# Optimization experiments

Measured on AMD Instinct MI355X. Metric: run time of the kernel, lower is better.

Reference implementation:

```python
import jax, jax.numpy as jnp
import numpy as np

NPOINT = 1024
K = 16
D_MODEL = 512
EPS = 1e-5


def _fps(xyz, npoint):
    # deterministic farthest point sampling (start at index 0)
    B, N, _ = xyz.shape
    def step(carry, _):
        dist, far = carry                                   # [B,N], [B]
        cent = jnp.take_along_axis(xyz, far[:, None, None], axis=1)  # [B,1,3]
        d = jnp.sum((xyz - cent) ** 2, axis=-1)             # [B,N]
        dist = jnp.minimum(dist, d)
        nxt = jnp.argmax(dist, axis=-1).astype(jnp.int32)
        return (dist, nxt), far
    init = (jnp.full((B, N), 1e10, xyz.dtype), jnp.zeros((B,), jnp.int32))
    _, idx = jax.lax.scan(step, init, None, length=npoint)
    return jnp.transpose(idx)                                # [B, npoint]


def _bn_relu(x, gamma, beta):
    # BatchNorm (training-mode batch stats, biased var) over all axes but channel-last
    axes = tuple(range(x.ndim - 1))
    mu = jnp.mean(x, axes, keepdims=True)
    var = jnp.var(x, axes, keepdims=True)
    return jax.nn.relu((x - mu) * jax.lax.rsqrt(var + EPS) * gamma + beta)


def _forward(xyz, feat, w1, b1, g1, bt1, fc1_w, fc1_b, wq, wk, wv, fc2_w, fc2_b,
             w2, b2, g2, bt2):
    B, N, C = feat.shape
    fps_idx = _fps(xyz, NPOINT)                              # [B,S]
    new_xyz = jnp.take_along_axis(xyz, fps_idx[:, :, None], axis=1)  # [B,S,3]
    # kNN of sampled centers against all points: squared distances [B,S,N]
    d = (jnp.sum(new_xyz ** 2, -1)[:, :, None]
         + jnp.sum(xyz ** 2, -1)[:, None, :]
         - 2.0 * jnp.einsum('bsc,bnc->bsn', new_xyz, xyz))
    _, knn_idx = jax.lax.top_k(-d, K)                        # [B,S,K]
    grouped = jnp.take_along_axis(
        feat, knn_idx.reshape(B, -1)[:, :, None], axis=1
    ).reshape(B, NPOINT, K, C)                               # [B,S,K,C]
    # mlp1: 1x1 conv + BN + ReLU (channel-last)
    x = _bn_relu(grouped @ w1.T + b1, g1, bt1)
    # TransformerBlock: local self-attention over the K neighbors
    pre = x
    h = x @ fc1_w.T + fc1_b                                  # [B,S,K,D]
    q, kk, v = h @ wq.T, h @ wk.T, h @ wv.T
    attn = jax.nn.softmax(
        jnp.einsum('bsnd,bsmd->bsnm', q, kk) / np.sqrt(D_MODEL), axis=-1)
    res = jnp.einsum('bsnm,bsmd->bsnd', attn, v)
    x = res @ fc2_w.T + fc2_b + pre                          # [B,S,K,C]
    # mlp2: 1x1 conv + BN + ReLU -> out_channel
    x = _bn_relu(x @ w2.T + b2, g2, bt2)                     # [B,S,K,out]
    new_feat = jnp.max(x, axis=2)                            # max-pool over neighbors
    return new_xyz, new_feat


def setup_inputs() -> dict:
    key = jax.random.key(0)
    ks = jax.random.split(key, 12)
    s = 0.02
    return {
        'xyz': jax.random.uniform(ks[0], (8, 4096, 3), jnp.float32),
        'feat': jax.random.normal(ks[1], (8, 4096, 64), jnp.float32),
        'w1': jax.random.normal(ks[2], (64, 64), jnp.float32) * s,
        'b1': jnp.zeros((64,), jnp.float32),
        'g1': jnp.ones((64,), jnp.float32),
        'bt1': jnp.zeros((64,), jnp.float32),
        'fc1_w': jax.random.normal(ks[3], (512, 64), jnp.float32) * s,
        'fc1_b': jnp.zeros((512,), jnp.float32),
        'wq': jax.random.normal(ks[4], (512, 512), jnp.float32) * s,
        'wk': jax.random.normal(ks[5], (512, 512), jnp.float32) * s,
        'wv': jax.random.normal(ks[6], (512, 512), jnp.float32) * s,
        'fc2_w': jax.random.normal(ks[7], (64, 512), jnp.float32) * s,
        'fc2_b': jnp.zeros((64,), jnp.float32),
        'w2': jax.random.normal(ks[8], (128, 64), jnp.float32) * s,
        'b2': jnp.zeros((128,), jnp.float32),
        'g2': jnp.ones((128,), jnp.float32),
        'bt2': jnp.zeros((128,), jnp.float32),
    }


def reference(xyz, feat, w1, b1, g1, bt1, fc1_w, fc1_b, wq, wk, wv, fc2_w, fc2_b,
              w2, b2, g2, bt2):
    return _forward(xyz, feat, w1, b1, g1, bt1, fc1_w, fc1_b, wq, wk, wv,
                    fc2_w, fc2_b, w2, b2, g2, bt2)
```

## Files before the change

kernel.cpp:

```cpp
#include <hip/hip_runtime.h>

#define EPSBN 1e-5f
#define INVSQ 0.04419417382415922f

#define WS_KNN_IDX   32768u
#define WS_X1        1048576u
#define WS_BNP1      34603008u
#define WS_BN1S      34865152u
#define WS_BNP2      34865664u
#define WS_BN2S      35914240u
#define WS_A         35915264u
#define WS_B         36046336u
#define WS_QB        36177408u
#define WS_KB        36179456u
#define WS_WC        36181504u
#define WS_G         36312576u
#define WS_ZT        36328960u
#define WS_U         36345344u
#define WS_W         36345600u
#define WS_TB        36345856u
#define WS_CC        36346112u
#define WS_PTS4      36346368u
#define WS_FPSPD     36870656u
#define WS_FPSC4     37001728u

__global__ __launch_bounds__(256) void pack_kernel(const float* __restrict__ xyz,
                                                   float4* __restrict__ pts4) {
  int id = blockIdx.x * 256 + threadIdx.x;
  float x = xyz[id * 3 + 0], y = xyz[id * 3 + 1], z = xyz[id * 3 + 2];
  float pp = __fadd_rn(__fadd_rn(__fmul_rn(x, x), __fmul_rn(y, y)), __fmul_rn(z, z));
  pts4[id] = make_float4(x, y, z, pp);
}

#define FPS_REDSTEP(CTRL)                                                              \
  {                                                                                    \
    unsigned lo2 = (unsigned)__builtin_amdgcn_update_dpp(0, (int)klo, CTRL, 0xF, 0xF, true); \
    unsigned hi2 = (unsigned)__builtin_amdgcn_update_dpp(0, (int)khi, CTRL, 0xF, 0xF, true); \
    bool tk = (hi2 > khi) || (hi2 == khi && lo2 > klo);                                \
    khi = tk ? hi2 : khi; klo = tk ? lo2 : klo;                                        \
  }

__device__ __forceinline__ void fps_chunk_body(unsigned char* smem, const float4* __restrict__ pts4,
                                               float* __restrict__ out_xyz,
                                               float* __restrict__ fps_pd,
                                               float4* __restrict__ fps_c4,
                                               int it0, int b, int t) {
  float4* spts = reinterpret_cast<float4*>(smem);
  float4* cent = reinterpret_cast<float4*>(smem + 65536);
  unsigned long long* red = reinterpret_cast<unsigned long long*>(smem + 73728);
  const int lane = t & 63, wid = t >> 6;
  const float4* pb = pts4 + (size_t)b * 4096;
  float px[16], py[16], pz[16], pd[16];
  if (it0 == 0) {
#pragma unroll
    for (int i = 0; i < 16; ++i) {
      int j = i * 256 + t;
      float4 p = pb[j];
      spts[j] = p;
      px[i] = p.x; py[i] = p.y; pz[i] = p.z; pd[i] = 1e10f;
    }
  } else {
#pragma unroll
    for (int i = 0; i < 16; ++i) {
      int j = i * 256 + t;
      float4 p = pb[j];
      spts[j] = p;
      px[i] = p.x; py[i] = p.y; pz[i] = p.z;
      pd[i] = fps_pd[i * 2048 + b * 256 + t];
    }
  }
  __syncthreads();
  float4 c4 = (it0 == 0) ? spts[0] : fps_c4[b];
  for (int it = it0; it < it0 + 512; ++it) {
    if (t == 0) cent[it - it0] = c4;
    float bv = -1.0f; int bj = 0;
#pragma unroll
    for (int i = 0; i < 16; ++i) {
      float dx = __fsub_rn(px[i], c4.x);
      float dy = __fsub_rn(py[i], c4.y);
      float dz = __fsub_rn(pz[i], c4.z);
      float d = __fadd_rn(__fadd_rn(__fmul_rn(dx, dx), __fmul_rn(dy, dy)), __fmul_rn(dz, dz));
      float nd = fminf(pd[i], d);
      pd[i] = nd;
      bool g = nd > bv;
      bv = g ? nd : bv;
      bj = g ? (i * 256 + t) : bj;
    }
    unsigned klo = 4095u - (unsigned)bj;
    unsigned khi = __float_as_uint(bv);
    FPS_REDSTEP(0x111)
    FPS_REDSTEP(0x112)
    FPS_REDSTEP(0x114)
    FPS_REDSTEP(0x118)
    FPS_REDSTEP(0x142)
    FPS_REDSTEP(0x143)
    unsigned wlo = (unsigned)__builtin_amdgcn_readlane((int)klo, 63);
    unsigned whi = (unsigned)__builtin_amdgcn_readlane((int)khi, 63);
    const int par = it & 1;
    if (lane == 0) red[par * 4 + wid] = (((unsigned long long)whi) << 32) | wlo;
    __syncthreads();
    const ulonglong2* r2 = reinterpret_cast<const ulonglong2*>(&red[par * 4]);
    ulonglong2 ka = r2[0];
    ulonglong2 kb2 = r2[1];
    unsigned long long m0 = (ka.x > ka.y) ? ka.x : ka.y;
    unsigned long long m1 = (kb2.x > kb2.y) ? kb2.x : kb2.y;
    unsigned long long k0 = (m0 > m1) ? m0 : m1;
    int jw = 4095 - (int)(unsigned)(k0 & 0xFFFFFFFFull);
    c4 = spts[jw];
  }
#pragma unroll
  for (int i = 0; i < 16; ++i) fps_pd[i * 2048 + b * 256 + t] = pd[i];
  if (t == 0) fps_c4[b] = c4;
  __syncthreads();
  for (int o = t; o < 1536; o += 256) {
    int j = o / 3;
    int c = o - 3 * j;
    out_xyz[(size_t)b * 3072 + (size_t)it0 * 3 + o] = (&cent[j].x)[c];
  }
}

__device__ __forceinline__ void knn_role_body(const float4* __restrict__ pts4,
                                              const float* __restrict__ out_xyz,
                                              int* __restrict__ knn_idx,
                                              int knn_c0, int blk, int t) {
  const int lane = t & 63;
  const int wv2 = (blk << 2) | (t >> 6);
  const int b = wv2 >> 9;
  const int center = b * 1024 + knn_c0 + (wv2 & 511);
  const float4* P = pts4 + (size_t)b * 4096;
  const float cx = out_xyz[(size_t)center * 3 + 0];
  const float cy = out_xyz[(size_t)center * 3 + 1];
  const float cz = out_xyz[(size_t)center * 3 + 2];
  const float cc2 = __fadd_rn(__fadd_rn(__fmul_rn(cx, cx), __fmul_rn(cy, cy)), __fmul_rn(cz, cz));
  float ldd[16]; int ldi[16];
#pragma unroll
  for (int q = 0; q < 16; ++q) { ldd[q] = 3.4e38f; ldi[q] = 0x7fffffff; }
  for (int i = 0; i < 64; ++i) {
    int j = i * 64 + lane;
    float4 p = P[j];
    float dot = __fadd_rn(__fadd_rn(__fmul_rn(cx, p.x), __fmul_rn(cy, p.y)), __fmul_rn(cz, p.z));
    float d = __fsub_rn(__fadd_rn(cc2, p.w), __fmul_rn(2.0f, dot));
    if (d < ldd[15] || (d == ldd[15] && j < ldi[15])) {
      float cd = d; int ci = j;
#pragma unroll
      for (int q = 0; q < 16; ++q) {
        bool sw = (cd < ldd[q]) || (cd == ldd[q] && ci < ldi[q]);
        float td = ldd[q]; int ti = ldi[q];
        if (sw) { ldd[q] = cd; ldi[q] = ci; cd = td; ci = ti; }
      }
    }
  }
  float cd = ldd[0]; int ci = ldi[0];
  int* op = knn_idx + (size_t)center * 16;
#pragma unroll 1
  for (int k = 0; k < 16; ++k) {
    float wd = cd; int wi = ci;
#pragma unroll
    for (int off = 1; off < 64; off <<= 1) {
      float ov = __shfl_xor(wd, off);
      int   oi = __shfl_xor(wi, off);
      bool tk = (ov < wd) || (ov == wd && oi < wi);
      wd = tk ? ov : wd; wi = tk ? oi : wi;
    }
    if (lane == 0) op[k] = wi;
    if (wd == cd && wi == ci) {
#pragma unroll
      for (int q = 0; q < 15; ++q) { ldd[q] = ldd[q + 1]; ldi[q] = ldi[q + 1]; }
      ldd[15] = 3.4e38f; ldi[15] = 0x7fffffff;
    }
    cd = ldd[0]; ci = ldi[0];
  }
}

__device__ __forceinline__ void mlp1_role_body(unsigned char* smem,
                                               const float* __restrict__ feat,
                                               const float* __restrict__ w1,
                                               const float* __restrict__ b1,
                                               const int* __restrict__ knn_idx,
                                               float* __restrict__ x1, float* __restrict__ bnp1,
                                               int mlp_c0, int blk, int t) {
  float* w1s = reinterpret_cast<float*>(smem);
  float* b1s = reinterpret_cast<float*>(smem + 16384);
  float (*ls)[64] = reinterpret_cast<float(*)[64]>(smem + 16640);
  float (*lq)[64] = reinterpret_cast<float(*)[64]>(smem + 17664);
  for (int i = t; i < 4096; i += 256) w1s[i] = w1[i];
  if (t < 64) b1s[t] = b1[t];
  __syncthreads();
  const int batch = blk >> 5;
  const size_t pbase = ((size_t)batch * 1024 + mlp_c0 + (blk & 31) * 16) * 16;
  const size_t pos = pbase + t;
  const int n = knn_idx[pos];
  const float4* fp = reinterpret_cast<const float4*>(feat + ((size_t)(batch * 4096 + n)) * 64);
  float4 fr[16];
#pragma unroll
  for (int i = 0; i < 16; ++i) fr[i] = fp[i];
  float4* op = reinterpret_cast<float4*>(x1 + pos * 64);
#pragma unroll
  for (int cq = 0; cq < 16; ++cq) {
    float a0 = b1s[cq * 4 + 0], a1 = b1s[cq * 4 + 1], a2 = b1s[cq * 4 + 2], a3 = b1s[cq * 4 + 3];
#pragma unroll
    for (int iq = 0; iq < 16; ++iq) {
      float4 f4 = fr[iq];
      float4 wa = *reinterpret_cast<const float4*>(&w1s[(cq * 4 + 0) * 64 + iq * 4]);
      float4 wb = *reinterpret_cast<const float4*>(&w1s[(cq * 4 + 1) * 64 + iq * 4]);
      float4 wc = *reinterpret_cast<const float4*>(&w1s[(cq * 4 + 2) * 64 + iq * 4]);
      float4 wd = *reinterpret_cast<const float4*>(&w1s[(cq * 4 + 3) * 64 + iq * 4]);
      a0 += f4.x * wa.x + f4.y * wa.y + f4.z * wa.z + f4.w * wa.w;
      a1 += f4.x * wb.x + f4.y * wb.y + f4.z * wb.z + f4.w * wb.w;
      a2 += f4.x * wc.x + f4.y * wc.y + f4.z * wc.z + f4.w * wc.w;
      a3 += f4.x * wd.x + f4.y * wd.y + f4.z * wd.z + f4.w * wd.w;
    }
    op[cq] = make_float4(a0, a1, a2, a3);
  }
  __threadfence_block();
  __syncthreads();
  {
    const int c2 = t & 63, g = t >> 6;
    const float* p = x1 + (pbase + g * 64) * 64 + c2;
    float s = 0.f, s2 = 0.f;
    for (int i = 0; i < 64; ++i) { float v = p[(size_t)i * 64]; s += v; s2 = fmaf(v, v, s2); }
    ls[g][c2] = s; lq[g][c2] = s2;
  }
  __syncthreads();
  if (t < 64) {
    const int slot = (mlp_c0 >> 9) * 256 + blk;
    bnp1[slot * 128 + t]      = ls[0][t] + ls[1][t] + ls[2][t] + ls[3][t];
    bnp1[slot * 128 + 64 + t] = lq[0][t] + lq[1][t] + lq[2][t] + lq[3][t];
  }
}

__global__ __launch_bounds__(256) void pipe_kernel(
    const float4* __restrict__ pts4, float* __restrict__ out_xyz,
    float* __restrict__ fps_pd, float4* __restrict__ fps_c4,
    int it0, int knn_c0, int prep_mode,
    int* __restrict__ knn_idx,
    const float* __restrict__ wq, const float* __restrict__ wk,
    const float* __restrict__ fc1w, const float* __restrict__ fc1b,
    const float* __restrict__ fc2w, const float* __restrict__ wv,
    const float* __restrict__ fc2b,
    float* __restrict__ A, float* __restrict__ B,
    float* __restrict__ qb, float* __restrict__ kb, float* __restrict__ Wc,
    float* __restrict__ G, float* __restrict__ u, float* __restrict__ w,
    float* __restrict__ cc, float* __restrict__ ZT, float* __restrict__ tb) {
  __shared__ __align__(16) unsigned char smem[73792];
  const int t = threadIdx.x;
  int base = 0;
  if (it0 >= 0) {
    if (blockIdx.x < 8) {
      fps_chunk_body(smem, pts4, out_xyz, fps_pd, fps_c4, it0, blockIdx.x, t);
      return;
    }
    base = 8;
  }
  if (knn_c0 >= 0) {
    if ((int)blockIdx.x < base + 1024) {
      knn_role_body(pts4, out_xyz, knn_idx, knn_c0, blockIdx.x - base, t);
      return;
    }
    base += 1024;
  }
  if (prep_mode == 1) {
    const int blk = blockIdx.x - base;
    if (blk < 256) {
      int id = blk * 256 + t;
      int which = id >> 15;
      int rem = id & 32767;
      int r = rem >> 6, i = rem & 63;
      const float* W = which ? wk : wq;
      float s = 0.f;
      for (int d = 0; d < 512; ++d) s = fmaf(W[r * 512 + d], fc1w[d * 64 + i], s);
      (which ? B : A)[r * 64 + i] = s;
      if (i == 0) {
        float sb = 0.f;
        for (int d = 0; d < 512; ++d) sb = fmaf(W[r * 512 + d], fc1b[d], sb);
        (which ? kb : qb)[r] = sb;
      }
    } else {
      int id = (blk - 256) * 256 + t;
      int c = id >> 9, d = id & 511;
      float s = 0.f;
      for (int e = 0; e < 512; ++e) s = fmaf(fc2w[c * 512 + e], wv[e * 512 + d], s);
      Wc[c * 512 + d] = s;
    }
  } else if (prep_mode == 2) {
    const int blk = blockIdx.x - base;
    if (blk < 17) {
      int id = blk * 256 + t;
      if (id < 4096) {
        int i = id >> 6, j = id & 63;
        float s = 0.f;
        for (int d = 0; d < 512; ++d) s = fmaf(A[d * 64 + i], B[d * 64 + j], s);
        G[i * 64 + j] = s * INVSQ;
      } else if (id < 4160) {
        int i = id - 4096; float s = 0.f;
        for (int d = 0; d < 512; ++d) s = fmaf(A[d * 64 + i], kb[d], s);
        u[i] = s * INVSQ;
      } else if (id < 4224) {
        int j = id - 4160; float s = 0.f;
        for (int d = 0; d < 512; ++d) s = fmaf(B[d * 64 + j], qb[d], s);
        w[j] = s * INVSQ;
      } else if (id == 4224) {
        float s = 0.f;
        for (int d = 0; d < 512; ++d) s = fmaf(qb[d], kb[d], s);
        cc[0] = s * INVSQ;
      }
    } else {
      int id = (blk - 17) * 256 + t;
      if (id < 4096) {
        int i = id >> 6, c = id & 63;
        float s = 0.f;
        for (int d = 0; d < 512; ++d) s = fmaf(Wc[c * 512 + d], fc1w[d * 64 + i], s);
        ZT[i * 64 + c] = s;
      } else if (id < 4160) {
        int c = id - 4096; float s = 0.f;
        for (int d = 0; d < 512; ++d) s = fmaf(Wc[c * 512 + d], fc1b[d], s);
        tb[c] = s + fc2b[c];
      }
    }
  }
}

__global__ __launch_bounds__(256) void tail_kernel(
    const float4* __restrict__ pts4, const float* __restrict__ out_xyz,
    int knn_c0, int mlp_c0,
    int* __restrict__ knn_idx,
    const float* __restrict__ feat, const float* __restrict__ w1,
    const float* __restrict__ b1, float* __restrict__ x1, float* __restrict__ bnp1) {
  __shared__ __align__(16) unsigned char smem[18688];
  const int t = threadIdx.x;
  int base = 0;
  if (knn_c0 >= 0) {
    if ((int)blockIdx.x < 1024) {
      knn_role_body(pts4, out_xyz, knn_idx, knn_c0, blockIdx.x, t);
      return;
    }
    base = 1024;
  }
  mlp1_role_body(smem, feat, w1, b1, knn_idx, x1, bnp1, mlp_c0, blockIdx.x - base, t);
}

__global__ __launch_bounds__(256) void bn1_final_kernel(const float* __restrict__ bnp1,
                                                        const float* __restrict__ g1,
                                                        const float* __restrict__ bt1,
                                                        float* __restrict__ bn1s) {
  __shared__ float rs[4][64], rq[4][64];
  const int t = threadIdx.x, c = t & 63, g = t >> 6;
  float S = 0.f, Q = 0.f;
  for (int i = g * 128; i < g * 128 + 128; ++i) {
    S += bnp1[i * 128 + c];
    Q += bnp1[i * 128 + 64 + c];
  }
  rs[g][c] = S; rq[g][c] = Q;
  __syncthreads();
  if (t < 64) {
    float Sa = rs[0][t] + rs[1][t] + rs[2][t] + rs[3][t];
    float Qa = rq[0][t] + rq[1][t] + rq[2][t] + rq[3][t];
    float m = Sa * (1.0f / 131072.0f);
    float var = Qa * (1.0f / 131072.0f) - m * m;
    float sc = g1[t] * rsqrtf(var + EPSBN);
    bn1s[t] = sc;
    bn1s[64 + t] = bt1[t] - m * sc;
  }
}

__global__ __launch_bounds__(64) void transformer_fused(
    float* __restrict__ x1, const float* __restrict__ bn1s,
    const float* __restrict__ G, const float* __restrict__ u, const float* __restrict__ w,
    const float* __restrict__ cc, const float* __restrict__ ZT, const float* __restrict__ tb) {
  __shared__ float pre[16][65];
  __shared__ float ts[16][65];
  __shared__ float ys[16][65];
  __shared__ float ss[16][17];
  __shared__ float spu[16], spw[16];
  const int c = threadIdx.x;
  const size_t base = (size_t)blockIdx.x * 1024;
  const float sc = bn1s[c], sh = bn1s[64 + c];
  float pc[16];
#pragma unroll
  for (int k = 0; k < 16; ++k) {
    float v = x1[base + k * 64 + c];
    float p = fmaxf(0.f, v * sc + sh);
    pc[k] = p; pre[k][c] = p;
  }
  __syncthreads();
  float tcol[16], ycol[16];
#pragma unroll
  for (int k = 0; k < 16; ++k) { tcol[k] = 0.f; ycol[k] = 0.f; }
  for (int i = 0; i < 64; ++i) {
    float g = G[i * 64 + c];
    float z = ZT[i * 64 + c];
#pragma unroll
    for (int k = 0; k < 16; ++k) {
      float p = pre[k][i];
      tcol[k] = fmaf(p, g, tcol[k]);
      ycol[k] = fmaf(p, z, ycol[k]);
    }
  }
#pragma unroll
  for (int k = 0; k < 16; ++k) { ts[k][c] = tcol[k]; ys[k][c] = ycol[k]; }
  if (c < 16) {
    float s = 0.f;
    for (int i = 0; i < 64; ++i) s = fmaf(pre[c][i], u[i], s);
    spu[c] = s;
  } else if (c < 32) {
    int m = c - 16; float s = 0.f;
    for (int i = 0; i < 64; ++i) s = fmaf(pre[m][i], w[i], s);
    spw[m] = s;
  }
  __syncthreads();
  {
    const float cval = cc[0];
    const int m = c & 15, nb = c >> 4;
#pragma unroll
    for (int ng = 0; ng < 4; ++ng) {
      int n = ng * 4 + nb;
      float s = 0.f;
      for (int i = 0; i < 64; ++i) s = fmaf(ts[n][i], pre[m][i], s);
      ss[n][m] = s + spu[n] + spw[m] + cval;
    }
  }
  __syncthreads();
  if (c < 16) {
    float mx = -3.4e38f;
#pragma unroll
    for (int m = 0; m < 16; ++m) mx = fmaxf(mx, ss[c][m]);
    float e[16], sum = 0.f;
#pragma unroll
    for (int m = 0; m < 16; ++m) { e[m] = expf(ss[c][m] - mx); sum += e[m]; }
    float r = 1.0f / sum;
#pragma unroll
    for (int m = 0; m < 16; ++m) ss[c][m] = e[m] * r;
  }
  __syncthreads();
  const float tbc = tb[c];
  float o[16];
#pragma unroll
  for (int k = 0; k < 16; ++k) o[k] = 0.f;
#pragma unroll
  for (int m = 0; m < 16; ++m) {
    float yv = ys[m][c];
#pragma unroll
    for (int k = 0; k < 16; ++k) o[k] = fmaf(ss[k][m], yv, o[k]);
  }
#pragma unroll
  for (int k = 0; k < 16; ++k) x1[base + k * 64 + c] = o[k] + tbc + pc[k];
}

__global__ __launch_bounds__(256) void bn2_stats_kernel(const float* __restrict__ x2,
                                                        const float* __restrict__ w2,
                                                        const float* __restrict__ b2,
                                                        float* __restrict__ bnp2,
                                                        float* __restrict__ out) {
  __shared__ float sx2[128 * 64];
  __shared__ float ps[2][128], pq[2][128];
  const int t = threadIdx.x;
  const float4* s4 = reinterpret_cast<const float4*>(x2 + (size_t)blockIdx.x * 128 * 64);
  float4* d4 = reinterpret_cast<float4*>(sx2);
  for (int i = 0; i < 8; ++i) d4[i * 256 + t] = s4[i * 256 + t];
  __syncthreads();
  const int c = t & 127, h = t >> 7;
  float4 wreg[16];
  const float4* w4 = reinterpret_cast<const float4*>(w2 + c * 64);
#pragma unroll
  for (int i = 0; i < 16; ++i) wreg[i] = w4[i];
  const float bb = b2[c];
  float s = 0.f, q = 0.f;
  float* omax = out + 24576 + ((size_t)blockIdx.x * 8 + 4 * h) * 128 + c;
#pragma unroll
  for (int gi = 0; gi < 4; ++gi) {
    float mx = -3.4e38f;
#pragma unroll 4
    for (int p2 = 0; p2 < 16; ++p2) {
      const int p = gi * 16 + p2;
      const float4* xr = reinterpret_cast<const float4*>(&sx2[(h * 64 + p) * 64]);
      float acc = bb;
#pragma unroll
      for (int i = 0; i < 16; ++i) {
        float4 xv = xr[i];
        acc += xv.x * wreg[i].x + xv.y * wreg[i].y + xv.z * wreg[i].z + xv.w * wreg[i].w;
      }
      s += acc; q = fmaf(acc, acc, q);
      mx = fmaxf(mx, acc);
    }
    omax[(size_t)gi * 128] = mx;
  }
  ps[h][c] = s; pq[h][c] = q;
  __syncthreads();
  if (t < 128) {
    bnp2[blockIdx.x * 256 + t]       = ps[0][t] + ps[1][t];
    bnp2[blockIdx.x * 256 + 128 + t] = pq[0][t] + pq[1][t];
  }
}

__global__ __launch_bounds__(512) void bn2_final_kernel(const float* __restrict__ bnp2,
                                                        const float* __restrict__ g2,
                                                        const float* __restrict__ bt2,
                                                        float* __restrict__ bn2s) {
  __shared__ float rs[4][128], rq[4][128];
  const int t = threadIdx.x, c = t & 127, g = t >> 7;
  float S = 0.f, Q = 0.f;
  for (int i = g * 256; i < g * 256 + 256; ++i) {
    S += bnp2[i * 256 + c];
    Q += bnp2[i * 256 + 128 + c];
  }
  rs[g][c] = S; rq[g][c] = Q;
  __syncthreads();
  if (t < 128) {
    float Sa = rs[0][t] + rs[1][t] + rs[2][t] + rs[3][t];
    float Qa = rq[0][t] + rq[1][t] + rq[2][t] + rq[3][t];
    float m = Sa * (1.0f / 131072.0f);
    float var = Qa * (1.0f / 131072.0f) - m * m;
    float sc = g2[t] * rsqrtf(var + EPSBN);
    bn2s[t] = sc;
    bn2s[128 + t] = bt2[t] - m * sc;
  }
}

__global__ __launch_bounds__(256) void final_kernel(const float* __restrict__ bn2s,
                                                    float* __restrict__ out) {
  __shared__ float s_sc[128], s_sh[128];
  const int t = threadIdx.x;
  if (t < 128) { s_sc[t] = bn2s[t]; s_sh[t] = bn2s[128 + t]; }
  __syncthreads();
  const int base = blockIdx.x * 1024 + t;
#pragma unroll
  for (int r = 0; r < 4; ++r) {
    const int i = base + r * 256;
    const int c = i & 127;
    float v = out[24576 + i];
    out[24576 + i] = fmaxf(0.f, v * s_sc[c] + s_sh[c]);
  }
}

extern "C" void kernel_launch(void* const* d_in, const int* in_sizes, int n_in,
                              void* d_out, int out_size, void* d_ws, size_t ws_size,
                              hipStream_t stream) {
  const float* xyz  = (const float*)d_in[0];
  const float* feat = (const float*)d_in[1];
  const float* w1   = (const float*)d_in[2];
  const float* b1   = (const float*)d_in[3];
  const float* g1   = (const float*)d_in[4];
  const float* bt1  = (const float*)d_in[5];
  const float* fc1w = (const float*)d_in[6];
  const float* fc1b = (const float*)d_in[7];
  const float* wq   = (const float*)d_in[8];
  const float* wk   = (const float*)d_in[9];
  const float* wv   = (const float*)d_in[10];
  const float* fc2w = (const float*)d_in[11];
  const float* fc2b = (const float*)d_in[12];
  const float* w2   = (const float*)d_in[13];
  const float* b2   = (const float*)d_in[14];
  const float* g2   = (const float*)d_in[15];
  const float* bt2  = (const float*)d_in[16];
  float* out = (float*)d_out;
  char* ws = (char*)d_ws;

  int*    knn_idx = (int*)(ws + WS_KNN_IDX);
  float*  x1      = (float*)(ws + WS_X1);
  float*  bnp1    = (float*)(ws + WS_BNP1);
  float*  bn1s    = (float*)(ws + WS_BN1S);
  float*  bnp2    = (float*)(ws + WS_BNP2);
  float*  bn2s    = (float*)(ws + WS_BN2S);
  float*  Abuf    = (float*)(ws + WS_A);
  float*  Bbuf    = (float*)(ws + WS_B);
  float*  qb      = (float*)(ws + WS_QB);
  float*  kb      = (float*)(ws + WS_KB);
  float*  Wc      = (float*)(ws + WS_WC);
  float*  G       = (float*)(ws + WS_G);
  float*  ZT      = (float*)(ws + WS_ZT);
  float*  u       = (float*)(ws + WS_U);
  float*  w       = (float*)(ws + WS_W);
  float*  tb      = (float*)(ws + WS_TB);
  float*  cc      = (float*)(ws + WS_CC);
  float4* pts4    = (float4*)(ws + WS_PTS4);
  float*  fps_pd  = (float*)(ws + WS_FPSPD);
  float4* fps_c4  = (float4*)(ws + WS_FPSC4);

#define PREP_ARGS wq, wk, fc1w, fc1b, fc2w, wv, fc2b, Abuf, Bbuf, qb, kb, Wc, G, u, w, cc, ZT, tb

  pack_kernel<<<128, 256, 0, stream>>>(xyz, pts4);
  pipe_kernel<<<392, 256, 0, stream>>>(pts4, out, fps_pd, fps_c4, 0, -1, 1,
                                       knn_idx, PREP_ARGS);
  pipe_kernel<<<1066, 256, 0, stream>>>(pts4, out, fps_pd, fps_c4, 512, 0, 2,
                                        knn_idx, PREP_ARGS);
  tail_kernel<<<1280, 256, 0, stream>>>(pts4, out, 512, 0, knn_idx, feat, w1, b1, x1, bnp1);
  tail_kernel<<<256, 256, 0, stream>>>(pts4, out, -1, 512, knn_idx, feat, w1, b1, x1, bnp1);
  bn1_final_kernel<<<1, 256, 0, stream>>>(bnp1, g1, bt1, bn1s);
  transformer_fused<<<8192, 64, 0, stream>>>(x1, bn1s, G, u, w, cc, ZT, tb);
  bn2_stats_kernel<<<1024, 256, 0, stream>>>(x1, w2, b2, bnp2, out);
  bn2_final_kernel<<<1, 512, 0, stream>>>(bnp2, g2, bt2, bn2s);
  final_kernel<<<1024, 256, 0, stream>>>(bn2s, out);
#undef PREP_ARGS
}
```

Measured before the change: 1.089 ms.

## Fuse mlp2 matmul and BN2 partial stats into the transformer kernel

The transformer kernel now applies the 64->128 mlp2 projection in place from shared memory. It computes per-group max and per-block sum and sum-of-squares directly, so the full transformer output no longer goes to global memory and gets read back by a separate stats kernel. Per-block partial stats are stashed in the x1 buffer and reduced by bn2_final. That reduction is a single block over 8192 partials instead of 1024, a much larger strided serial reduction that could offset the bandwidth saved.

```diff
diff --git a/kernel.cpp b/kernel.cpp
--- a/kernel.cpp
+++ b/kernel.cpp
@@ -6,9 +6,8 @@
 #define WS_KNN_IDX   32768u
 #define WS_X1        1048576u
 #define WS_BNP1      34603008u
-#define WS_BN1S      34865152u
-#define WS_BNP2      34865664u
-#define WS_BN2S      35914240u
+#define WS_BN1S      35127296u
+#define WS_BN2S      35127808u
 #define WS_A         35915264u
 #define WS_B         36046336u
 #define WS_QB        36177408u
@@ -363,10 +362,12 @@
   }
 }
 
-__global__ __launch_bounds__(64) void transformer_fused(
+__global__ __launch_bounds__(64) void transformer_bn2_kernel(
     float* __restrict__ x1, const float* __restrict__ bn1s,
     const float* __restrict__ G, const float* __restrict__ u, const float* __restrict__ w,
-    const float* __restrict__ cc, const float* __restrict__ ZT, const float* __restrict__ tb) {
+    const float* __restrict__ cc, const float* __restrict__ ZT, const float* __restrict__ tb,
+    const float* __restrict__ w2, const float* __restrict__ b2,
+    float* __restrict__ out) {
   __shared__ float pre[16][65];
   __shared__ float ts[16][65];
   __shared__ float ys[16][65];
@@ -443,65 +444,50 @@
     for (int k = 0; k < 16; ++k) o[k] = fmaf(ss[k][m], yv, o[k]);
   }
 #pragma unroll
-  for (int k = 0; k < 16; ++k) x1[base + k * 64 + c] = o[k] + tbc + pc[k];
-}
-
-__global__ __launch_bounds__(256) void bn2_stats_kernel(const float* __restrict__ x2,
-                                                        const float* __restrict__ w2,
-                                                        const float* __restrict__ b2,
-                                                        float* __restrict__ bnp2,
-                                                        float* __restrict__ out) {
-  __shared__ float sx2[128 * 64];
-  __shared__ float ps[2][128], pq[2][128];
-  const int t = threadIdx.x;
-  const float4* s4 = reinterpret_cast<const float4*>(x2 + (size_t)blockIdx.x * 128 * 64);
-  float4* d4 = reinterpret_cast<float4*>(sx2);
-  for (int i = 0; i < 8; ++i) d4[i * 256 + t] = s4[i * 256 + t];
-  __syncthreads();
-  const int c = t & 127, h = t >> 7;
-  float4 wreg[16];
-  const float4* w4 = reinterpret_cast<const float4*>(w2 + c * 64);
-#pragma unroll
-  for (int i = 0; i < 16; ++i) wreg[i] = w4[i];
-  const float bb = b2[c];
-  float s = 0.f, q = 0.f;
-  float* omax = out + 24576 + ((size_t)blockIdx.x * 8 + 4 * h) * 128 + c;
-#pragma unroll
-  for (int gi = 0; gi < 4; ++gi) {
-    float mx = -3.4e38f;
-#pragma unroll 4
-    for (int p2 = 0; p2 < 16; ++p2) {
-      const int p = gi * 16 + p2;
-      const float4* xr = reinterpret_cast<const float4*>(&sx2[(h * 64 + p) * 64]);
-      float acc = bb;
-#pragma unroll
-      for (int i = 0; i < 16; ++i) {
-        float4 xv = xr[i];
-        acc += xv.x * wreg[i].x + xv.y * wreg[i].y + xv.z * wreg[i].z + xv.w * wreg[i].w;
-      }
-      s += acc; q = fmaf(acc, acc, q);
-      mx = fmaxf(mx, acc);
-    }
-    omax[(size_t)gi * 128] = mx;
-  }
-  ps[h][c] = s; pq[h][c] = q;
-  __syncthreads();
-  if (t < 128) {
-    bnp2[blockIdx.x * 256 + t]       = ps[0][t] + ps[1][t];
-    bnp2[blockIdx.x * 256 + 128 + t] = pq[0][t] + pq[1][t];
-  }
-}
-
-__global__ __launch_bounds__(512) void bn2_final_kernel(const float* __restrict__ bnp2,
+  for (int k = 0; k < 16; ++k) pre[k][c] = o[k] + tbc + pc[k];
+  __syncthreads();
+  float acc0[16], acc1[16];
+#pragma unroll
+  for (int k = 0; k < 16; ++k) { acc0[k] = 0.f; acc1[k] = 0.f; }
+  const int ch0 = c, ch1 = c + 64;
+  for (int iq = 0; iq < 16; ++iq) {
+    float4 wa = *reinterpret_cast<const float4*>(&w2[ch0 * 64 + iq * 4]);
+    float4 wb = *reinterpret_cast<const float4*>(&w2[ch1 * 64 + iq * 4]);
+#pragma unroll
+    for (int k = 0; k < 16; ++k) {
+      float4 xv = *reinterpret_cast<const float4*>(&pre[k][iq * 4]);
+      acc0[k] += xv.x * wa.x + xv.y * wa.y + xv.z * wa.z + xv.w * wa.w;
+      acc1[k] += xv.x * wb.x + xv.y * wb.y + xv.z * wb.z + xv.w * wb.w;
+    }
+  }
+  const float bb0 = b2[ch0], bb1 = b2[ch1];
+  float s0 = 0.f, q0 = 0.f, mx0 = -3.4e38f;
+  float s1 = 0.f, q1 = 0.f, mx1 = -3.4e38f;
+#pragma unroll
+  for (int k = 0; k < 16; ++k) {
+    float v0 = bb0 + acc0[k];
+    float v1 = bb1 + acc1[k];
+    s0 += v0; q0 = fmaf(v0, v0, q0); mx0 = fmaxf(mx0, v0);
+    s1 += v1; q1 = fmaf(v1, v1, q1); mx1 = fmaxf(mx1, v1);
+  }
+  out[24576 + (size_t)blockIdx.x * 128 + ch0] = mx0;
+  out[24576 + (size_t)blockIdx.x * 128 + ch1] = mx1;
+  x1[base + ch0] = s0;
+  x1[base + ch1] = s1;
+  x1[base + 128 + ch0] = q0;
+  x1[base + 128 + ch1] = q1;
+}
+
+__global__ __launch_bounds__(512) void bn2_final_kernel(const float* __restrict__ x1,
                                                         const float* __restrict__ g2,
                                                         const float* __restrict__ bt2,
                                                         float* __restrict__ bn2s) {
   __shared__ float rs[4][128], rq[4][128];
   const int t = threadIdx.x, c = t & 127, g = t >> 7;
   float S = 0.f, Q = 0.f;
-  for (int i = g * 256; i < g * 256 + 256; ++i) {
-    S += bnp2[i * 256 + c];
-    Q += bnp2[i * 256 + 128 + c];
+  for (int i = g * 2048; i < g * 2048 + 2048; ++i) {
+    S += x1[(size_t)i * 1024 + c];
+    Q += x1[(size_t)i * 1024 + 128 + c];
   }
   rs[g][c] = S; rq[g][c] = Q;
   __syncthreads();
@@ -559,7 +545,6 @@
   float*  x1      = (float*)(ws + WS_X1);
   float*  bnp1    = (float*)(ws + WS_BNP1);
   float*  bn1s    = (float*)(ws + WS_BN1S);
-  float*  bnp2    = (float*)(ws + WS_BNP2);
   float*  bn2s    = (float*)(ws + WS_BN2S);
   float*  Abuf    = (float*)(ws + WS_A);
   float*  Bbuf    = (float*)(ws + WS_B);
@@ -586,9 +571,8 @@
   tail_kernel<<<1280, 256, 0, stream>>>(pts4, out, 512, 0, knn_idx, feat, w1, b1, x1, bnp1);
   tail_kernel<<<256, 256, 0, stream>>>(pts4, out, -1, 512, knn_idx, feat, w1, b1, x1, bnp1);
   bn1_final_kernel<<<1, 256, 0, stream>>>(bnp1, g1, bt1, bn1s);
-  transformer_fused<<<8192, 64, 0, stream>>>(x1, bn1s, G, u, w, cc, ZT, tb);
-  bn2_stats_kernel<<<1024, 256, 0, stream>>>(x1, w2, b2, bnp2, out);
-  bn2_final_kernel<<<1, 512, 0, stream>>>(bnp2, g2, bt2, bn2s);
+  transformer_bn2_kernel<<<8192, 64, 0, stream>>>(x1, bn1s, G, u, w, cc, ZT, tb, w2, b2, out);
+  bn2_final_kernel<<<1, 512, 0, stream>>>(x1, g2, bt2, bn2s);
   final_kernel<<<1024, 256, 0, stream>>>(bn2s, out);
 #undef PREP_ARGS
 }
```

New measurement: 1.134 ms. +4.2%, slower.
